# Kernel optimization log

Measured on AMD Instinct MI355X. Metric: run time of the kernel, lower is better.

## Reference

```python
import jax, jax.numpy as jnp
import numpy as np

NSMP = 8192
NA = 512  # min_in_features
DOUT = 256  # out_features
REALNA = 520  # input.shape[1] - nSmp


def setup_inputs() -> dict:
    key = jax.random.key(0)
    k1, k2 = jax.random.split(key)
    inp = jax.random.uniform(k1, (NSMP, REALNA + NSMP), dtype=jnp.float32)
    weight = jax.random.uniform(k2, (NA, DOUT), dtype=jnp.float32)  # torch.rand init
    return {"input": inp, "weight": weight}


def reference(input, weight):
    nSmp = NSMP
    na = NA
    X = input[:, :na]  # [nSmp, na]
    realna = input.shape[1] - nSmp
    A = input[:, realna - 8:realna + nSmp - 8]  # [nSmp, nSmp]
    A = A + jnp.eye(nSmp, dtype=input.dtype)
    # D = diag(colsum(A)); D_hat = inverse(D)**0.5 == diag(d^{-1/2})
    d = jnp.sum(A, axis=0)
    d_inv_sqrt = jax.lax.rsqrt(d)
    # DAD = D_hat @ A @ D_hat, applied as row/col scaling (exploits diagonal structure)
    DAD = d_inv_sqrt[:, None] * A * d_inv_sqrt[None, :]
    support = X @ weight  # [nSmp, out]
    output = DAD @ support  # [nSmp, out]
    # bias=False in init, so no bias add
    return jnp.concatenate((output, A), axis=1)  # [nSmp, out + nSmp]
```

## Files before the change

kernel.cpp:

```cpp
#include <hip/hip_runtime.h>

#define NSMP 8192
#define INW  8712
#define OUTW 8448
#define AOFF 512
#define DO   256

typedef __attribute__((ext_vector_type(4)))  float f32x4;
typedef __attribute__((ext_vector_type(8)))  short short8;
typedef __attribute__((ext_vector_type(16))) float floatx16;

typedef __attribute__((address_space(1))) const unsigned int* gptr_t;
typedef __attribute__((address_space(3)))       unsigned int* lptr_t;

__device__ __forceinline__ unsigned pk_bf16(float lo, float hi) {
    return (__float_as_uint(lo) >> 16) | (__float_as_uint(hi) & 0xffff0000u);
}

__device__ __forceinline__ void gload_lds16(const void* g, void* l) {
    __builtin_amdgcn_global_load_lds((gptr_t)g, (lptr_t)l, 16, 0, 0);
}

__global__ __launch_bounds__(256) void kcopy(const float* __restrict__ in,
                                             float* __restrict__ out,
                                             float* __restrict__ d,
                                             unsigned short* __restrict__ aP) {
    const int t  = threadIdx.x;
    const int j0 = blockIdx.x * 1024;
    const int i0 = blockIdx.y * 32;
    const int jc = j0 + 4 * t;
    const float*    src = in  + (size_t)i0 * INW  + AOFF + jc;
    float*          dst = out + (size_t)i0 * OUTW + DO   + jc;
    unsigned short* ap  = aP  + (size_t)i0 * NSMP + jc;
    f32x4 cs = {0.f, 0.f, 0.f, 0.f};
#pragma unroll 8
    for (int r = 0; r < 32; ++r) {
        f32x4 v = __builtin_nontemporal_load((const f32x4*)(src + (size_t)r * INW));
        uint2 pb;
        pb.x = pk_bf16(v[0], v[1]);
        pb.y = pk_bf16(v[2], v[3]);
        *(uint2*)(ap + (size_t)r * NSMP) = pb;
        int di = (i0 + r) - j0;
        if ((di >> 2) == t) {
            int s = di & 3;
            v[0] += (s == 0); v[1] += (s == 1); v[2] += (s == 2); v[3] += (s == 3);
        }
        cs += v;
        __builtin_nontemporal_store(v, (f32x4*)(dst + (size_t)r * OUTW));
    }
    atomicAdd(&d[jc + 0], cs[0]);
    atomicAdd(&d[jc + 1], cs[1]);
    atomicAdd(&d[jc + 2], cs[2]);
    atomicAdd(&d[jc + 3], cs[3]);
}

__global__ __launch_bounds__(256) void ksupport(const float* __restrict__ in,
                                                const float* __restrict__ w,
                                                const float* __restrict__ d,
                                                float* __restrict__ dinv,
                                                unsigned short* __restrict__ sP) {
    const int c  = threadIdx.x;
    const int r0 = blockIdx.x * 8;
    const float* X = in + (size_t)r0 * INW;
    float acc[8] = {0.f, 0.f, 0.f, 0.f, 0.f, 0.f, 0.f, 0.f};
#pragma unroll 4
    for (int k = 0; k < 512; ++k) {
        float wv = w[(size_t)k * DO + c];
#pragma unroll
        for (int r = 0; r < 8; ++r)
            acc[r] = fmaf(X[(size_t)r * INW + k], wv, acc[r]);
    }
    union { unsigned short h[8]; uint4 u; } pk;
#pragma unroll
    for (int r = 0; r < 8; ++r) {
        float dv = rsqrtf(d[r0 + r]);
        unsigned ub = __float_as_uint(acc[r] * dv);
        ub += 0x7fffu + ((ub >> 16) & 1u);
        pk.h[r] = (unsigned short)(ub >> 16);
    }
    *(uint4*)(sP + (size_t)(r0 >> 3) * (DO * 8) + (size_t)c * 8) = pk.u;
    if (c < 8) dinv[r0 + c] = rsqrtf(d[r0 + c]);
}

__global__ __launch_bounds__(256, 2) void kmm(const unsigned short* __restrict__ aP,
                                              const unsigned short* __restrict__ sP,
                                              const float* __restrict__ dinv,
                                              float* __restrict__ out) {
    __shared__ __align__(16) unsigned short lA[2][32 * 64];

    const int b  = blockIdx.x;
    const int rg = ((b >> 4) << 3) + (b & 7);
    const int ch = (b >> 3) & 1;
    const int tid = threadIdx.x;
    const int w = tid >> 6, lane = tid & 63;
    const int m = lane & 31, q = lane >> 5;
    const int i0 = rg * 32;
    const int cc = ch * 128 + w * 32 + m;

    const int srow = lane >> 3;
    const int sg   = lane & 7;
    const unsigned short* aSrc = aP + (size_t)(i0 + w * 8 + srow) * NSMP
                                    + 8 * (sg ^ (srow & 7));
    const unsigned short* bB   = sP + (size_t)q * 2048 + (size_t)cc * 8;

    floatx16 acc;
#pragma unroll
    for (int z = 0; z < 16; ++z) acc[z] = 0.f;

    uint4 Ba0, Ba1, Ba2, Ba3, Bb0, Bb1, Bb2, Bb3;

#define STAGE_A(nb, s) gload_lds16(aSrc + (size_t)(s) * 64, &lA[nb][w * 512])
#define LOAD_B(P, s) do {                                              \
        P##0 = *(const uint4*)(bB + (size_t)((s) * 8 + 0) * 2048);     \
        P##1 = *(const uint4*)(bB + (size_t)((s) * 8 + 2) * 2048);     \
        P##2 = *(const uint4*)(bB + (size_t)((s) * 8 + 4) * 2048);     \
        P##3 = *(const uint4*)(bB + (size_t)((s) * 8 + 6) * 2048);     \
    } while (0)
#define MFMA_KS(cur, Breg, ks) do {                                    \
        union { uint4 u; short8 s8; } fb_; fb_.u = Breg;               \
        const short8 af_ = *(const short8*)(                           \
            &lA[cur][m * 64 + ((((ks) * 2 + q) ^ (m & 7)) * 8)]);      \
        acc = __builtin_amdgcn_mfma_f32_32x32x16_bf16(af_, fb_.s8, acc, 0, 0, 0); \
    } while (0)
#define COMPUTE(cur, P) do {                                           \
        MFMA_KS(cur, P##0, 0); MFMA_KS(cur, P##1, 1);                  \
        MFMA_KS(cur, P##2, 2); MFMA_KS(cur, P##3, 3);                  \
    } while (0)

    STAGE_A(0, 0);
    LOAD_B(Ba, 0);
    __syncthreads();

    for (int s = 0; s < 128; s += 2) {
        STAGE_A(1, s + 1);
        LOAD_B(Bb, s + 1);
        COMPUTE(0, Ba);
        __syncthreads();
        const int s2 = (s + 2 < 128) ? s + 2 : 0;
        STAGE_A(0, s2);
        LOAD_B(Ba, s2);
        COMPUTE(1, Bb);
        __syncthreads();
    }

#undef STAGE_A
#undef LOAD_B
#undef MFMA_KS
#undef COMPUTE

#pragma unroll
    for (int g = 0; g < 4; ++g) {
        const ushort4 s4 = *(const ushort4*)(sP + (size_t)(i0 / 8 + g) * (DO * 8)
                                                + (size_t)cc * 8 + 4 * q);
        unsigned short sv[4] = {s4.x, s4.y, s4.z, s4.w};
#pragma unroll
        for (int rr = 0; rr < 4; ++rr) {
            const int row = i0 + 8 * g + 4 * q + rr;
            const float idt = __uint_as_float(((unsigned)sv[rr]) << 16);
            out[(size_t)row * OUTW + cc] = (acc[g * 4 + rr] + idt) * dinv[row];
        }
    }
}

extern "C" void kernel_launch(void* const* d_in, const int* in_sizes, int n_in,
                              void* d_out, int out_size, void* d_ws, size_t ws_size,
                              hipStream_t stream) {
    (void)in_sizes; (void)n_in; (void)out_size; (void)ws_size;
    const float* in = (const float*)d_in[0];
    const float* w  = (const float*)d_in[1];
    float* out  = (float*)d_out;
    float* d    = (float*)d_ws;
    float* dinv = d + NSMP;
    unsigned short* sP = (unsigned short*)(d + 2 * NSMP);
    unsigned short* aP = sP + (size_t)1024 * DO * 8;

    hipMemsetAsync(d, 0, NSMP * sizeof(float), stream);
    kcopy<<<dim3(8, 256), 256, 0, stream>>>(in, out, d, aP);
    ksupport<<<1024, 256, 0, stream>>>(in, w, d, dinv, sP);
    kmm<<<512, 256, 0, stream>>>(aP, sP, dinv, out);
}
```

Baseline: 624.1 us.

## Stage B tiles through LDS with triple-buffered async pipeline in kmm

The matmul kernel now loads the support (B) operand into shared memory with direct global-to-LDS loads instead of into registers, and moves from a double-buffered to a triple-buffered ring. Each iteration waits on a partial vmcnt plus a barrier rather than a full syncthreads, which keeps two stages of loads in flight while computing. It also raises wave priority around the MFMA block. The cost is more LDS per block, which may reduce occupancy, and correctness now relies on the hand-written vmcnt count.

```diff
diff --git a/kernel.cpp b/kernel.cpp
--- a/kernel.cpp
+++ b/kernel.cpp
@@ -86,7 +86,8 @@
                                               const unsigned short* __restrict__ sP,
                                               const float* __restrict__ dinv,
                                               float* __restrict__ out) {
-    __shared__ __align__(16) unsigned short lA[2][32 * 64];
+    __shared__ __align__(16) unsigned short lA[3][32 * 64];
+    __shared__ __align__(16) unsigned short lB[3][8 * 128 * 8];
 
     const int b  = blockIdx.x;
     const int rg = ((b >> 4) << 3) + (b & 7);
@@ -101,51 +102,49 @@
     const int sg   = lane & 7;
     const unsigned short* aSrc = aP + (size_t)(i0 + w * 8 + srow) * NSMP
                                     + 8 * (sg ^ (srow & 7));
-    const unsigned short* bB   = sP + (size_t)q * 2048 + (size_t)cc * 8;
+    const unsigned short* bSrc = sP + (size_t)(ch * 128 + lane) * 8;
 
     floatx16 acc;
 #pragma unroll
     for (int z = 0; z < 16; ++z) acc[z] = 0.f;
 
-    uint4 Ba0, Ba1, Ba2, Ba3, Bb0, Bb1, Bb2, Bb3;
-
-#define STAGE_A(nb, s) gload_lds16(aSrc + (size_t)(s) * 64, &lA[nb][w * 512])
-#define LOAD_B(P, s) do {                                              \
-        P##0 = *(const uint4*)(bB + (size_t)((s) * 8 + 0) * 2048);     \
-        P##1 = *(const uint4*)(bB + (size_t)((s) * 8 + 2) * 2048);     \
-        P##2 = *(const uint4*)(bB + (size_t)((s) * 8 + 4) * 2048);     \
-        P##3 = *(const uint4*)(bB + (size_t)((s) * 8 + 6) * 2048);     \
-    } while (0)
-#define MFMA_KS(cur, Breg, ks) do {                                    \
-        union { uint4 u; short8 s8; } fb_; fb_.u = Breg;               \
-        const short8 af_ = *(const short8*)(                           \
-            &lA[cur][m * 64 + ((((ks) * 2 + q) ^ (m & 7)) * 8)]);      \
-        acc = __builtin_amdgcn_mfma_f32_32x32x16_bf16(af_, fb_.s8, acc, 0, 0, 0); \
-    } while (0)
-#define COMPUTE(cur, P) do {                                           \
-        MFMA_KS(cur, P##0, 0); MFMA_KS(cur, P##1, 1);                  \
-        MFMA_KS(cur, P##2, 2); MFMA_KS(cur, P##3, 3);                  \
+#define STAGE(buf, t) do {                                                     \
+        const int O0_ = (t) * 8 + w;                                           \
+        gload_lds16(aSrc + (size_t)(t) * 64,            &lA[buf][w * 512]);    \
+        gload_lds16(bSrc + (size_t)O0_ * 2048,          &lB[buf][w * 1024]);   \
+        gload_lds16(bSrc + (size_t)O0_ * 2048 + 512,    &lB[buf][w * 1024 + 512]); \
+        gload_lds16(bSrc + (size_t)(O0_ + 4) * 2048,       &lB[buf][(w + 4) * 1024]); \
+        gload_lds16(bSrc + (size_t)(O0_ + 4) * 2048 + 512, &lB[buf][(w + 4) * 1024 + 512]); \
     } while (0)
 
-    STAGE_A(0, 0);
-    LOAD_B(Ba, 0);
-    __syncthreads();
+#define COMPUTE(buf) do {                                                      \
+        const unsigned short* lAc_ = &lA[buf][0];                              \
+        const unsigned short* lBc_ = &lB[buf][0];                              \
+        _Pragma("unroll")                                                      \
+        for (int ks = 0; ks < 4; ++ks) {                                       \
+            const short8 af_ = *(const short8*)(                               \
+                lAc_ + m * 64 + (((ks * 2 + q) ^ (m & 7)) * 8));               \
+            const short8 bf_ = *(const short8*)(                               \
+                lBc_ + (2 * ks + q) * 1024 + (w * 32 + m) * 8);                \
+            acc = __builtin_amdgcn_mfma_f32_32x32x16_bf16(af_, bf_, acc, 0, 0, 0); \
+        }                                                                      \
+    } while (0)
 
-    for (int s = 0; s < 128; s += 2) {
-        STAGE_A(1, s + 1);
-        LOAD_B(Bb, s + 1);
-        COMPUTE(0, Ba);
-        __syncthreads();
-        const int s2 = (s + 2 < 128) ? s + 2 : 0;
-        STAGE_A(0, s2);
-        LOAD_B(Ba, s2);
-        COMPUTE(1, Bb);
-        __syncthreads();
+    STAGE(0, 0);
+    STAGE(1, 1);
+
+    int rd = 0, wr = 2;
+    for (int s = 0; s < 128; ++s) {
+        asm volatile("s_waitcnt vmcnt(5)\n\ts_barrier" ::: "memory");
+        STAGE(wr, (s + 2) & 127);
+        __builtin_amdgcn_s_setprio(1);
+        COMPUTE(rd);
+        __builtin_amdgcn_s_setprio(0);
+        rd = (rd == 2) ? 0 : rd + 1;
+        wr = (wr == 2) ? 0 : wr + 1;
     }
 
-#undef STAGE_A
-#undef LOAD_B
-#undef MFMA_KS
+#undef STAGE
 #undef COMPUTE
 
 #pragma unroll
```

Result: no change. 633.9 us (+1.6%).

## Triple-buffer A tiles in LDS with manual vmcnt waits and MFMA priority

Applied to the files above, without the earlier changes.

The main GEMM loop moves from a double-buffered LDS tile with two full __syncthreads per step to a three-stage ring buffer that prefetches two tiles ahead. Each step waits on a partial vmcnt before one s_barrier and raises wave priority around the MFMA block. The aim is to hide global-load latency and cut barrier stalls. The hand-counted vmcnt(5) depends on exact instruction ordering, so a compiler reordering loads could break correctness, and the extra LDS buffer may reduce occupancy.

```diff
diff --git a/kernel.cpp b/kernel.cpp
--- a/kernel.cpp
+++ b/kernel.cpp
@@ -86,7 +86,7 @@
                                               const unsigned short* __restrict__ sP,
                                               const float* __restrict__ dinv,
                                               float* __restrict__ out) {
-    __shared__ __align__(16) unsigned short lA[2][32 * 64];
+    __shared__ __align__(16) unsigned short lA[3][32 * 64];
 
     const int b  = blockIdx.x;
     const int rg = ((b >> 4) << 3) + (b & 7);
@@ -127,20 +127,30 @@
         MFMA_KS(cur, P##2, 2); MFMA_KS(cur, P##3, 3);                  \
     } while (0)
 
-    STAGE_A(0, 0);
-    LOAD_B(Ba, 0);
-    __syncthreads();
+    STAGE_A(0, 0);  LOAD_B(Ba, 0);
+    STAGE_A(1, 1);  LOAD_B(Bb, 1);
 
+    int rd = 0, wr = 2;
     for (int s = 0; s < 128; s += 2) {
-        STAGE_A(1, s + 1);
-        LOAD_B(Bb, s + 1);
-        COMPUTE(0, Ba);
-        __syncthreads();
-        const int s2 = (s + 2 < 128) ? s + 2 : 0;
-        STAGE_A(0, s2);
-        LOAD_B(Ba, s2);
-        COMPUTE(1, Bb);
-        __syncthreads();
+        asm volatile("s_waitcnt vmcnt(5)" ::: "memory");
+        __builtin_amdgcn_s_barrier();
+        STAGE_A(wr, (s + 2) & 127);
+        __builtin_amdgcn_s_setprio(1);
+        COMPUTE(rd, Ba);
+        __builtin_amdgcn_s_setprio(0);
+        LOAD_B(Ba, (s + 2) & 127);
+        rd = (rd == 2) ? 0 : rd + 1;
+        wr = (wr == 2) ? 0 : wr + 1;
+
+        asm volatile("s_waitcnt vmcnt(5)" ::: "memory");
+        __builtin_amdgcn_s_barrier();
+        STAGE_A(wr, (s + 3) & 127);
+        __builtin_amdgcn_s_setprio(1);
+        COMPUTE(rd, Bb);
+        __builtin_amdgcn_s_setprio(0);
+        LOAD_B(Bb, (s + 3) & 127);
+        rd = (rd == 2) ? 0 : rd + 1;
+        wr = (wr == 2) ? 0 : wr + 1;
     }
 
 #undef STAGE_A
```

New measurement: 611.6 us. -2.0%, faster.
